# Optimization experiments

Hardware: AMD Instinct MI355X
Metric: run time of the kernel (lower is better)

The kernel has to match this reference:

```python
import jax, jax.numpy as jnp
import numpy as np

H = 16
D = 1024
DK = D // H


def setup_inputs() -> dict:
    key = jax.random.key(0)
    ks = jax.random.split(key, 10)
    B, S = 2, 2048
    scale = 1.0 / np.sqrt(D)
    inp = {
        "query": jax.random.normal(ks[0], (B, S, D), jnp.float32),
        "key_": jax.random.normal(ks[1], (B, S, D), jnp.float32),
        "value": jax.random.normal(ks[2], (B, S, D), jnp.float32),
        "Wq": jax.random.normal(ks[3], (D, D), jnp.float32) * scale,
        "bq": jnp.zeros((D,), jnp.float32),
        "Wk": jax.random.normal(ks[4], (D, D), jnp.float32) * scale,
        "bk": jnp.zeros((D,), jnp.float32),
        "Wv": jax.random.normal(ks[5], (D, D), jnp.float32) * scale,
        "bv": jnp.zeros((D,), jnp.float32),
        "ln_gamma": jnp.ones((D,), jnp.float32),
        "ln_beta": jnp.zeros((D,), jnp.float32),
    }
    return inp


def reference(query, key_, value, Wq, bq, Wk, bk, Wv, bv, ln_gamma, ln_beta):
    B, S, _ = query.shape
    residual = query
    # projections, split into heads: [B, H, S, DK]
    def proj(x, W, b):
        return (x @ W + b).reshape(B, -1, H, DK).transpose(0, 2, 1, 3)
    q = proj(query, Wq, bq)
    k = proj(key_, Wk, bk)
    v = proj(value, Wv, bv)
    # scaled dot-product attention with full score matrix (as in source)
    scores = jnp.einsum("bhqd,bhkd->bhqk", q, k) / jnp.sqrt(jnp.float32(DK))
    p_att = jax.nn.softmax(scores, axis=-1)  # dropout p=0 -> identity
    x = jnp.einsum("bhqk,bhkd->bhqd", p_att, v)
    x = x.transpose(0, 2, 1, 3).reshape(B, S, D)
    # residual + LayerNorm(eps=1e-6)
    y = x + residual
    mu = jnp.mean(y, axis=-1, keepdims=True)
    var = jnp.var(y, axis=-1, keepdims=True)
    y = (y - mu) / jnp.sqrt(var + 1e-6)
    return y * ln_gamma + ln_beta
```

## Files before the change

### kernel.cpp

```cpp
#include <hip/hip_runtime.h>


typedef float f32x4 __attribute__((ext_vector_type(4)));
typedef short short8 __attribute__((ext_vector_type(8)));
typedef unsigned int uint32x2 __attribute__((ext_vector_type(2)));

__device__ __forceinline__ unsigned short f2bf(float f) {
    unsigned u = __builtin_bit_cast(unsigned, f);
    u += 0x7fffu + ((u >> 16) & 1u);
    return (unsigned short)(u >> 16);
}
__device__ __forceinline__ unsigned packbf2(float lo, float hi) {
    return __builtin_amdgcn_perm(__builtin_bit_cast(unsigned, hi),
                                 __builtin_bit_cast(unsigned, lo), 0x07060302u);
}

__device__ __forceinline__ void g2l16(const unsigned short* g, unsigned short* l) {
    __builtin_amdgcn_global_load_lds(
        (const __attribute__((address_space(1))) unsigned int*)g,
        (__attribute__((address_space(3))) unsigned int*)l, 16, 0, 0);
}

__global__ __launch_bounds__(256) void convert_x(
    const float* __restrict__ xq, const float* __restrict__ xk, const float* __restrict__ xv,
    unsigned short* __restrict__ out)
{
    const int z = blockIdx.z;
    const float* src = (z == 0) ? xq : (z == 1) ? xk : xv;
    const size_t idx = ((size_t)blockIdx.x * 256 + threadIdx.x) * 8;
    const float4 a = *(const float4*)(src + idx);
    const float4 b = *(const float4*)(src + idx + 4);
    short8 o;
    o[0] = (short)f2bf(a.x); o[1] = (short)f2bf(a.y);
    o[2] = (short)f2bf(a.z); o[3] = (short)f2bf(a.w);
    o[4] = (short)f2bf(b.x); o[5] = (short)f2bf(b.y);
    o[6] = (short)f2bf(b.z); o[7] = (short)f2bf(b.w);
    *(short8*)(out + (size_t)z * 4194304 + idx) = o;
}

__global__ __launch_bounds__(256) void convert_wt(
    const float* __restrict__ Wq, const float* __restrict__ Wk, const float* __restrict__ Wv,
    unsigned short* __restrict__ out)
{
    const int z = blockIdx.z;
    const float* W = (z == 0) ? Wq : (z == 1) ? Wk : Wv;
    unsigned short* Wt = out + (size_t)z * 1048576;

    __shared__ unsigned short Ts[64 * 65];
    const int tid = threadIdx.x;
    const int kb0 = blockIdx.x * 64, nb0 = blockIdx.y * 64;
    const int a = tid >> 6, b = tid & 63;

#pragma unroll
    for (int i = 0; i < 16; ++i) {
        const int k = i * 4 + a, n = b;
        Ts[n * 65 + k] = f2bf(W[(size_t)(kb0 + k) * 1024 + nb0 + n]);
    }
    __syncthreads();
#pragma unroll
    for (int i = 0; i < 16; ++i) {
        const int n = i * 4 + a, k = b;
        Wt[(size_t)(nb0 + n) * 1024 + kb0 + k] = Ts[n * 65 + k];
    }
}

__global__ __launch_bounds__(256) void qkv_gemm(
    const unsigned short* __restrict__ Xb, const unsigned short* __restrict__ Wtb,
    const float* __restrict__ bq, const float* __restrict__ bk, const float* __restrict__ bv,
    unsigned short* __restrict__ qo, unsigned short* __restrict__ ko, unsigned short* __restrict__ vo)
{
    const int z = blockIdx.z;
    const unsigned short* X  = Xb  + (size_t)z * 4194304;
    const unsigned short* Wt = Wtb + (size_t)z * 1048576;
    const float* bias   = (z == 0) ? bq : (z == 1) ? bk : bv;
    unsigned short* out = (z == 0) ? qo : (z == 1) ? ko : vo;

    __shared__ unsigned short smem[8192];
    unsigned short* As = smem;
    unsigned short* Bs = smem + 4096;

    const int tid  = threadIdx.x;
    const int wave = tid >> 6;
    const int lane = tid & 63;
    const int l15  = lane & 15;
    const int quad = lane >> 4;
    const int mq   = wave & 1, nq = wave >> 1;
    const int mbase = blockIdx.x * 128, nbase = blockIdx.y * 128;

    const int srow = lane >> 2;
    const int schk = (lane & 3) ^ (srow & 3);

    f32x4 acc[4][4];
#pragma unroll
    for (int i = 0; i < 4; ++i)
#pragma unroll
        for (int j = 0; j < 4; ++j) acc[i][j] = (f32x4){0.f, 0.f, 0.f, 0.f};

    for (int k0 = 0; k0 < 1024; k0 += 32) {
        __syncthreads();
#pragma unroll
        for (int t = 0; t < 2; ++t) {
            const int row = wave * 32 + t * 16 + srow;
            g2l16(X  + (size_t)(mbase + row) * 1024 + k0 + schk * 8, &As[(wave * 32 + t * 16) * 32]);
            g2l16(Wt + (size_t)(nbase + row) * 1024 + k0 + schk * 8, &Bs[(wave * 32 + t * 16) * 32]);
        }
        __syncthreads();

        short8 af[4], bf[4];
#pragma unroll
        for (int i = 0; i < 4; ++i) {
            af[i] = *(const short8*)(&As[(mq * 64 + i * 16 + l15) * 32 + ((quad ^ (l15 & 3)) << 3)]);
            bf[i] = *(const short8*)(&Bs[(nq * 64 + i * 16 + l15) * 32 + ((quad ^ (l15 & 3)) << 3)]);
        }
#pragma unroll
        for (int mt = 0; mt < 4; ++mt)
#pragma unroll
            for (int nt = 0; nt < 4; ++nt)
                acc[mt][nt] = __builtin_amdgcn_mfma_f32_16x16x32_bf16(af[mt], bf[nt], acc[mt][nt], 0, 0, 0);
    }

    __syncthreads();

    float bvals[4];
#pragma unroll
    for (int nt = 0; nt < 4; ++nt) bvals[nt] = bias[nbase + nq * 64 + nt * 16 + l15];

    if (z == 2) {
        unsigned short* Epv = smem;
        const int hbase = nbase >> 6;
        const int b     = mbase >> 11;
        const int srow0 = mbase & 2047;
#pragma unroll
        for (int nt = 0; nt < 4; ++nt) {
            __syncthreads();
            short8 w[2];
#pragma unroll
            for (int e = 0; e < 2; ++e)
#pragma unroll
                for (int j = 0; j < 8; ++j) {
                    const int idx = e * 8 + j, mt2 = idx & 3, r = idx >> 2;
                    w[e][j] = (short)f2bf(acc[mt2][nt][r] + bvals[nt]);
                }
            unsigned short* dst = &Epv[(nq * 16 + l15) * 136 + mq * 64 + quad * 16];
            *(short8*)(dst)     = w[0];
            *(short8*)(dst + 8) = w[1];
            __syncthreads();
            const int row = tid >> 3;
            const int d   = nt * 16 + (row & 15);
            const int h   = hbase + (row >> 4);
#pragma unroll
            for (int e = 0; e < 2; ++e) {
                const int colb = e * 64 + (tid & 7) * 8;
                short8 v = *(const short8*)(&Epv[row * 136 + colb]);
                *(short8*)(&out[((size_t)(b * 16 + h) * 64 + d) * 2048 + srow0 + colb]) = v;
            }
        }
    } else {
        unsigned short* Ep = smem + wave * 1152;
        const int hQ = (nbase + nq * 64) >> 6;
        const float scl = (z == 0) ? 0.18033688f : 1.0f;
#pragma unroll
        for (int mt = 0; mt < 4; ++mt) {
#pragma unroll
            for (int nt = 0; nt < 4; ++nt)
#pragma unroll
                for (int r = 0; r < 4; ++r)
                    Ep[(quad * 4 + r) * 72 + nt * 16 + l15] =
                        f2bf((acc[mt][nt][r] + bvals[nt]) * scl);
#pragma unroll
            for (int half = 0; half < 2; ++half) {
                const int m = (lane >> 3) + half * 8;
                const int nblk = lane & 7;
                short8 v = *(const short8*)(&Ep[m * 72 + nblk * 8]);
                const int gm = mbase + mq * 64 + mt * 16 + m;
                const int b2 = gm >> 11, srw = gm & 2047;
                *(short8*)(&out[((size_t)(b2 * 16 + hQ) * 2048 + srw) * 64 + nblk * 8]) = v;
            }
        }
    }
}

__global__ __launch_bounds__(256) void attn(
    const unsigned short* __restrict__ qb, const unsigned short* __restrict__ kb,
    const unsigned short* __restrict__ vtb, float* __restrict__ xw)
{
    const int tid  = threadIdx.x;
    const int wave = tid >> 6;
    const int lane = tid & 63;
    const int l15  = lane & 15;
    const int quad = lane >> 4;

    const int bh    = blockIdx.x;
    const int qbase = blockIdx.y * 128 + wave * 32;

    __shared__ unsigned short Ks[64 * 64];
    __shared__ unsigned short Vs[64 * 64];
    __shared__ unsigned short Pt[4][2][16][72];

    short8 qf[2][2];
#pragma unroll
    for (int mt = 0; mt < 2; ++mt) {
        const unsigned short* Qp = qb + ((size_t)bh * 2048 + qbase + mt * 16 + l15) * 64 + quad * 8;
        qf[mt][0] = *(const short8*)(Qp);
        qf[mt][1] = *(const short8*)(Qp + 32);
    }

    const unsigned short* Kbh = kb  + (size_t)bh * 2048 * 64;
    const unsigned short* Vbh = vtb + (size_t)bh * 64 * 2048;

    const int r8 = lane >> 3, c8 = lane & 7;
    const unsigned short *srcK[2], *srcV[2];
    unsigned short *dstK[2], *dstV[2];
#pragma unroll
    for (int t = 0; t < 2; ++t) {
        const int row = wave * 16 + t * 8 + r8;
        srcK[t] = Kbh + (size_t)row * 64   + ((c8 ^ r8) << 3);
        srcV[t] = Vbh + (size_t)row * 2048 + ((c8 ^ r8) << 3);
        dstK[t] = &Ks[(wave * 16 + t * 8) * 64];
        dstV[t] = &Vs[(wave * 16 + t * 8) * 64];
    }

    float l_r[2][4] = {{0.f,0.f,0.f,0.f},{0.f,0.f,0.f,0.f}};
    f32x4 O[2][4];
#pragma unroll
    for (int mt = 0; mt < 2; ++mt)
#pragma unroll
        for (int i = 0; i < 4; ++i) O[mt][i] = (f32x4){0.f, 0.f, 0.f, 0.f};

    for (int kt = 0; kt < 2048; kt += 64) {
        __syncthreads();
#pragma unroll
        for (int t = 0; t < 2; ++t) {
            g2l16(srcK[t] + (size_t)kt * 64, dstK[t]);
            g2l16(srcV[t] + kt,              dstV[t]);
        }
        __syncthreads();

        short8 kf[4][2];
#pragma unroll
        for (int ct = 0; ct < 4; ++ct)
#pragma unroll
            for (int kk = 0; kk < 2; ++kk)
                kf[ct][kk] = *(const short8*)(&Ks[(ct * 16 + l15) * 64 +
                                                  ((((kk << 2) + quad) ^ (l15 & 7)) << 3)]);

#pragma unroll
        for (int mt = 0; mt < 2; ++mt) {
            f32x4 sc[4];
#pragma unroll
            for (int ct = 0; ct < 4; ++ct) {
                f32x4 a = {0.f, 0.f, 0.f, 0.f};
                a = __builtin_amdgcn_mfma_f32_16x16x32_bf16(qf[mt][0], kf[ct][0], a, 0, 0, 0);
                a = __builtin_amdgcn_mfma_f32_16x16x32_bf16(qf[mt][1], kf[ct][1], a, 0, 0, 0);
                sc[ct] = a;
            }
#pragma unroll
            for (int r = 0; r < 4; ++r) {
                const float p0 = __builtin_amdgcn_exp2f(sc[0][r]);
                const float p1 = __builtin_amdgcn_exp2f(sc[1][r]);
                const float p2 = __builtin_amdgcn_exp2f(sc[2][r]);
                const float p3 = __builtin_amdgcn_exp2f(sc[3][r]);
                l_r[mt][r] += (p0 + p1) + (p2 + p3);
                uint32x2 pk = {packbf2(p0, p1), packbf2(p2, p3)};
                *(uint32x2*)(&Pt[wave][mt][quad * 4 + r][l15 * 4]) = pk;
            }
        }

#pragma unroll
        for (int c = 0; c < 2; ++c) {
            const short8 pf0 = *(const short8*)(&Pt[wave][0][l15][c * 32 + quad * 8]);
            const short8 pf1 = *(const short8*)(&Pt[wave][1][l15][c * 32 + quad * 8]);
#pragma unroll
            for (int ct4 = 0; ct4 < 4; ++ct4) {
                const short8 vf = *(const short8*)(&Vs[(ct4 * 16 + l15) * 64 +
                                                       ((((c << 2) + quad) ^ (l15 & 7)) << 3)]);
                O[0][ct4] = __builtin_amdgcn_mfma_f32_16x16x32_bf16(pf0, vf, O[0][ct4], 0, 0, 0);
                O[1][ct4] = __builtin_amdgcn_mfma_f32_16x16x32_bf16(pf1, vf, O[1][ct4], 0, 0, 0);
            }
        }
    }

    float inv[2][4];
#pragma unroll
    for (int mt = 0; mt < 2; ++mt)
#pragma unroll
        for (int r = 0; r < 4; ++r) {
            float s = l_r[mt][r];
#pragma unroll
            for (int off = 8; off >= 1; off >>= 1) s += __shfl_xor(s, off);
            inv[mt][r] = 1.0f / s;
        }

    const int b = bh >> 4, h = bh & 15;
#pragma unroll
    for (int mt = 0; mt < 2; ++mt)
#pragma unroll
        for (int ct4 = 0; ct4 < 4; ++ct4)
#pragma unroll
            for (int r = 0; r < 4; ++r) {
                const int s = qbase + mt * 16 + quad * 4 + r;
                xw[((size_t)b * 2048 + s) * 1024 + h * 64 + ct4 * 16 + l15] =
                    O[mt][ct4][r] * inv[mt][r];
            }
}

__global__ __launch_bounds__(256) void ln_kernel(
    const float* __restrict__ xw, const float* __restrict__ res,
    const float* __restrict__ gamma, const float* __restrict__ beta,
    float* __restrict__ out)
{
    const int row = blockIdx.x;
    const int tid = threadIdx.x;
    const size_t base = (size_t)row * 1024 + tid * 4;

    const float4 x  = *(const float4*)(xw + base);
    const float4 rv = *(const float4*)(res + base);
    float4 y;
    y.x = x.x + rv.x; y.y = x.y + rv.y; y.z = x.z + rv.z; y.w = x.w + rv.w;

    float s  = y.x + y.y + y.z + y.w;
    float s2 = y.x * y.x + y.y * y.y + y.z * y.z + y.w * y.w;
#pragma unroll
    for (int off = 32; off >= 1; off >>= 1) {
        s  += __shfl_xor(s, off);
        s2 += __shfl_xor(s2, off);
    }
    __shared__ float red[8];
    const int wave = tid >> 6;
    if ((tid & 63) == 0) { red[wave] = s; red[4 + wave] = s2; }
    __syncthreads();
    s  = red[0] + red[1] + red[2] + red[3];
    s2 = red[4] + red[5] + red[6] + red[7];

    const float mu   = s * (1.0f / 1024.0f);
    const float var  = s2 * (1.0f / 1024.0f) - mu * mu;
    const float rstd = rsqrtf(var + 1e-6f);

    const float4 g  = *(const float4*)(gamma + tid * 4);
    const float4 bt = *(const float4*)(beta + tid * 4);
    float4 o;
    o.x = (y.x - mu) * rstd * g.x + bt.x;
    o.y = (y.y - mu) * rstd * g.y + bt.y;
    o.z = (y.z - mu) * rstd * g.z + bt.z;
    o.w = (y.w - mu) * rstd * g.w + bt.w;
    *(float4*)(out + base) = o;
}

extern "C" void kernel_launch(void* const* d_in, const int* in_sizes, int n_in,
                              void* d_out, int out_size, void* d_ws, size_t ws_size,
                              hipStream_t stream) {
    const float* query = (const float*)d_in[0];
    const float* key_  = (const float*)d_in[1];
    const float* value = (const float*)d_in[2];
    const float* Wq    = (const float*)d_in[3];
    const float* bq    = (const float*)d_in[4];
    const float* Wk    = (const float*)d_in[5];
    const float* bk    = (const float*)d_in[6];
    const float* Wv    = (const float*)d_in[7];
    const float* bv    = (const float*)d_in[8];
    const float* ln_g  = (const float*)d_in[9];
    const float* ln_b  = (const float*)d_in[10];
    float* out = (float*)d_out;

    char* ws = (char*)d_ws;
    unsigned short* Xbuf = (unsigned short*)(ws);
    float*          xwp  = (float*)(ws);
    unsigned short* Wtb  = (unsigned short*)(ws + (size_t)24 * 1024 * 1024);
    unsigned short* qbuf = (unsigned short*)(ws + (size_t)30 * 1024 * 1024);
    unsigned short* kbuf = (unsigned short*)(ws + (size_t)38 * 1024 * 1024);
    unsigned short* vtb  = (unsigned short*)(ws + (size_t)46 * 1024 * 1024);

    convert_x <<<dim3(2048, 1, 3), 256, 0, stream>>>(query, key_, value, Xbuf);
    convert_wt<<<dim3(16, 16, 3),  256, 0, stream>>>(Wq, Wk, Wv, Wtb);
    qkv_gemm  <<<dim3(32, 8, 3),   256, 0, stream>>>(Xbuf, Wtb, bq, bk, bv, qbuf, kbuf, vtb);
    attn      <<<dim3(32, 16),     256, 0, stream>>>(qbuf, kbuf, vtb, xwp);
    ln_kernel <<<4096,             256, 0, stream>>>(xwp, query, ln_g, ln_b, out);
}
```

Before: 225.9 us.

## Split attention key range across two blocks and merge partials in LayerNorm

The attention grid gains a z dimension that splits the 2048 keys into two halves, so twice as many blocks run. Each block writes its unnormalised partial output and row sums to workspace. The LayerNorm kernel then adds the two partials, divides by the combined sum, and applies the residual and normalisation. This is meant to raise parallelism and latency hiding in the attention kernel, at the cost of an extra fp32 partial-output buffer that must be written and read back.

```diff
diff --git a/kernel.cpp b/kernel.cpp
--- a/kernel.cpp
+++ b/kernel.cpp
@@ -182,7 +182,8 @@
 
 __global__ __launch_bounds__(256) void attn(
     const unsigned short* __restrict__ qb, const unsigned short* __restrict__ kb,
-    const unsigned short* __restrict__ vtb, float* __restrict__ xw)
+    const unsigned short* __restrict__ vtb, float* __restrict__ o_ws,
+    float* __restrict__ l_ws)
 {
     const int tid  = threadIdx.x;
     const int wave = tid >> 6;
@@ -192,6 +193,7 @@
 
     const int bh    = blockIdx.x;
     const int qbase = blockIdx.y * 128 + wave * 32;
+    const int zk    = blockIdx.z;
 
     __shared__ unsigned short Ks[64 * 64];
     __shared__ unsigned short Vs[64 * 64];
@@ -227,7 +229,8 @@
 #pragma unroll
         for (int i = 0; i < 4; ++i) O[mt][i] = (f32x4){0.f, 0.f, 0.f, 0.f};
 
-    for (int kt = 0; kt < 2048; kt += 64) {
+    for (int it = 0; it < 16; ++it) {
+        const int kt = zk * 1024 + it * 64;
         __syncthreads();
 #pragma unroll
         for (int t = 0; t < 2; ++t) {
@@ -280,7 +283,7 @@
         }
     }
 
-    float inv[2][4];
+    float lsum[2][4];
 #pragma unroll
     for (int mt = 0; mt < 2; ++mt)
 #pragma unroll
@@ -288,9 +291,18 @@
             float s = l_r[mt][r];
 #pragma unroll
             for (int off = 8; off >= 1; off >>= 1) s += __shfl_xor(s, off);
-            inv[mt][r] = 1.0f / s;
-        }
-
+            lsum[mt][r] = s;
+        }
+    if (l15 == 0) {
+        float* lp = l_ws + ((size_t)zk * 32 + bh) * 2048;
+#pragma unroll
+        for (int mt = 0; mt < 2; ++mt)
+#pragma unroll
+            for (int r = 0; r < 4; ++r)
+                lp[qbase + mt * 16 + quad * 4 + r] = lsum[mt][r];
+    }
+
+    float* xo = o_ws + (size_t)zk * 4194304;
     const int b = bh >> 4, h = bh & 15;
 #pragma unroll
     for (int mt = 0; mt < 2; ++mt)
@@ -299,40 +311,49 @@
 #pragma unroll
             for (int r = 0; r < 4; ++r) {
                 const int s = qbase + mt * 16 + quad * 4 + r;
-                xw[((size_t)b * 2048 + s) * 1024 + h * 64 + ct4 * 16 + l15] =
-                    O[mt][ct4][r] * inv[mt][r];
+                xo[((size_t)b * 2048 + s) * 1024 + h * 64 + ct4 * 16 + l15] = O[mt][ct4][r];
             }
 }
 
 __global__ __launch_bounds__(256) void ln_kernel(
-    const float* __restrict__ xw, const float* __restrict__ res,
+    const float* __restrict__ o_ws, const float* __restrict__ l_ws,
+    const float* __restrict__ res,
     const float* __restrict__ gamma, const float* __restrict__ beta,
     float* __restrict__ out)
 {
     const int row = blockIdx.x;
     const int tid = threadIdx.x;
     const size_t base = (size_t)row * 1024 + tid * 4;
-
-    const float4 x  = *(const float4*)(xw + base);
+    const int b = row >> 11, s = row & 2047, h = tid >> 4;
+
+    const float4 o1 = *(const float4*)(o_ws + base);
+    const float4 o2 = *(const float4*)(o_ws + 4194304 + base);
+    const float  l1 = l_ws[(size_t)(b * 16 + h) * 2048 + s];
+    const float  l2 = l_ws[(size_t)(32 + b * 16 + h) * 2048 + s];
+    const float inv = 1.0f / (l1 + l2);
     const float4 rv = *(const float4*)(res + base);
+
     float4 y;
-    y.x = x.x + rv.x; y.y = x.y + rv.y; y.z = x.z + rv.z; y.w = x.w + rv.w;
-
-    float s  = y.x + y.y + y.z + y.w;
+    y.x = (o1.x + o2.x) * inv + rv.x;
+    y.y = (o1.y + o2.y) * inv + rv.y;
+    y.z = (o1.z + o2.z) * inv + rv.z;
+    y.w = (o1.w + o2.w) * inv + rv.w;
+
+    float sm  = y.x + y.y + y.z + y.w;
     float s2 = y.x * y.x + y.y * y.y + y.z * y.z + y.w * y.w;
 #pragma unroll
     for (int off = 32; off >= 1; off >>= 1) {
-        s  += __shfl_xor(s, off);
+        sm += __shfl_xor(sm, off);
         s2 += __shfl_xor(s2, off);
     }
     __shared__ float red[8];
     const int wave = tid >> 6;
-    if ((tid & 63) == 0) { red[wave] = s; red[4 + wave] = s2; }
+    if ((tid & 63) == 0) { red[wave] = sm; red[4 + wave] = s2; }
     __syncthreads();
-    s  = red[0] + red[1] + red[2] + red[3];
+    sm = red[0] + red[1] + red[2] + red[3];
     s2 = red[4] + red[5] + red[6] + red[7];
 
-    const float mu   = s * (1.0f / 1024.0f);
+    const float mu   = sm * (1.0f / 1024.0f);
     const float var  = s2 * (1.0f / 1024.0f) - mu * mu;
     const float rstd = rsqrtf(var + 1e-6f);
 
@@ -362,17 +383,19 @@
     const float* ln_b  = (const float*)d_in[10];
     float* out = (float*)d_out;
 
+    const size_t MB = 1024 * 1024;
     char* ws = (char*)d_ws;
+    float*          o_ws = (float*)(ws);
     unsigned short* Xbuf = (unsigned short*)(ws);
-    float*          xwp  = (float*)(ws);
-    unsigned short* Wtb  = (unsigned short*)(ws + (size_t)24 * 1024 * 1024);
-    unsigned short* qbuf = (unsigned short*)(ws + (size_t)30 * 1024 * 1024);
-    unsigned short* kbuf = (unsigned short*)(ws + (size_t)38 * 1024 * 1024);
-    unsigned short* vtb  = (unsigned short*)(ws + (size_t)46 * 1024 * 1024);
+    unsigned short* Wtb  = (unsigned short*)(ws + 24 * MB);
+    float*          l_ws = (float*)(ws + 32 * MB);
+    unsigned short* qbuf = (unsigned short*)(ws + 33 * MB);
+    unsigned short* kbuf = (unsigned short*)(ws + 41 * MB);
+    unsigned short* vtb  = (unsigned short*)(ws + 49 * MB);
 
     convert_x <<<dim3(2048, 1, 3), 256, 0, stream>>>(query, key_, value, Xbuf);
     convert_wt<<<dim3(16, 16, 3),  256, 0, stream>>>(Wq, Wk, Wv, Wtb);
     qkv_gemm  <<<dim3(32, 8, 3),   256, 0, stream>>>(Xbuf, Wtb, bq, bk, bv, qbuf, kbuf, vtb);
-    attn      <<<dim3(32, 16),     256, 0, stream>>>(qbuf, kbuf, vtb, xwp);
-    ln_kernel <<<4096,             256, 0, stream>>>(xwp, query, ln_g, ln_b, out);
-}
+    attn      <<<dim3(32, 16, 2),  256, 0, stream>>>(qbuf, kbuf, vtb, o_ws, l_ws);
+    ln_kernel <<<4096,             256, 0, stream>>>(o_ws, l_ws, query, ln_g, ln_b, out);
+}
```

Result: slower. 231.3 us (+2.4%).
